# Kernel tuning notes

Hardware: AMD Instinct MI355X
Metric: run time of the kernel (lower is better)

The kernel has to match this reference:

```python
import jax, jax.numpy as jnp
import numpy as np

N = 250000          # number of points (also used as padded #unique voxels)
EPS = 1e-5          # BatchNorm1d eps
DIMS = [9, 64, 128, 256, 64]
PROJ = 16


def _bn(x, g, b):
    # torch BatchNorm1d in training mode: biased batch var
    m = jnp.mean(x, axis=0)
    v = jnp.var(x, axis=0)
    return (x - m) * jax.lax.rsqrt(v + EPS) * g + b


def setup_inputs() -> dict:
    key = jax.random.key(0)
    ks = list(jax.random.split(key, 24))
    inp = {
        "feats": jax.random.normal(ks[0], (N, DIMS[0]), jnp.float32),
        "coords": jax.random.randint(ks[1], (N, 3), 0, 48, jnp.int32),
    }
    k = 2
    # 4 BatchNorms over dims 9, 64, 128, 256
    for i, d in enumerate(DIMS[:4]):
        inp[f"bn{i}_g"] = jnp.ones((d,), jnp.float32)
        inp[f"bn{i}_b"] = jnp.zeros((d,), jnp.float32)
    # 4 Linear layers 9->64->128->256->64, stored as [in, out]
    for i in range(4):
        fin, fout = DIMS[i], DIMS[i + 1]
        inp[f"w{i+1}"] = jax.random.normal(ks[k], (fin, fout), jnp.float32) * (1.0 / np.sqrt(fin)); k += 1
        inp[f"b{i+1}"] = jnp.zeros((fout,), jnp.float32)
    # feature projection 64 -> 16 (kaiming-ish init, bias 0.01)
    inp["wp"] = jax.random.normal(ks[k], (DIMS[4], PROJ), jnp.float32) * np.sqrt(2.0 / PROJ); k += 1
    inp["bp"] = jnp.full((PROJ,), 0.01, jnp.float32)
    return inp


def reference(feats, coords, bn0_g, bn0_b, bn1_g, bn1_b, bn2_g, bn2_b, bn3_g, bn3_b,
              w1, b1, w2, b2, w3, b3, w4, b4, wp, bp):
    # unique voxel coords (sorted rows, like torch.unique dim=0); padded to N for jit
    unq, inv, cnt = jnp.unique(coords, axis=0, return_inverse=True, return_counts=True,
                               size=N, fill_value=-1)
    inv = inv.reshape(-1)

    # point MLP: BN -> Lin -> BN -> ReLU -> Lin -> BN -> ReLU -> Lin -> BN -> ReLU -> Lin
    x = _bn(feats, bn0_g, bn0_b)
    x = jax.nn.relu(_bn(x @ w1 + b1, bn1_g, bn1_b))
    x = jax.nn.relu(_bn(x @ w2 + b2, bn2_g, bn2_b))
    x = jax.nn.relu(_bn(x @ w3 + b3, bn3_g, bn3_b))
    x = x @ w4 + b4                                   # [N, 64]

    # scatter_max pooling per voxel; empty (padding) segments zeroed
    pooled = jax.ops.segment_max(x, inv, num_segments=N)
    pooled = jnp.where((cnt > 0)[:, None], pooled, 0.0)

    # feature projection + ReLU
    pooled = jax.nn.relu(pooled @ wp + bp)            # [N, 16] (rows >= #unique are padding)
    return pooled, unq.astype(jnp.int32)
```

## Files before the change

### kernel.cpp

```cpp
#include <hip/hip_runtime.h>
#include <hip/hip_bf16.h>

#define EPSBN 1e-5f
#define NKEYS 110592
#define SLICES 64
#define VPW 8

typedef __attribute__((ext_vector_type(8))) short bf16x8;
typedef __attribute__((ext_vector_type(4))) float f32x4;

__device__ __forceinline__ float bf2f(ushort u){ return __uint_as_float(((unsigned)u)<<16); }
__device__ __forceinline__ ushort f2bf(float f){
  unsigned u = __float_as_uint(f);
  unsigned r = u + 0x7fffu + ((u>>16)&1u);
  return (ushort)(r>>16);
}

template<int KP>
__device__ __forceinline__ int swz(int row, int kbyte){
  constexpr int MASK = (KP >= 64) ? 7 : 3;
  return row*(KP*2) + (kbyte ^ ((row & MASK) << 4));
}

__device__ __forceinline__ int tri(int k, int l){
  if (k > l){ int t=k; k=l; l=t; }
  return k*9 - (k*(k-1))/2 + (l-k);
}

__global__ __launch_bounds__(256) void k_zero(uint4* __restrict__ p, size_t n16){
  size_t i = (size_t)blockIdx.x*256 + threadIdx.x;
  size_t stride = (size_t)gridDim.x*256;
  uint4 z = make_uint4(0,0,0,0);
  for (; i < n16; i += stride) p[i] = z;
}

__global__ __launch_bounds__(256) void k_wprep(const float* __restrict__ w,
    ushort* __restrict__ wf, int K, int M){
  int CT = M >> 4;
  int KS = (K + 31) >> 5;
  int total = KS*CT*512;
  for (int idx = blockIdx.x*256 + threadIdx.x; idx < total; idx += gridDim.x*256){
    int e = idx & 7, l = (idx>>3) & 63, c = idx >> 9;
    int ct = c % CT, ks = c / CT;
    int g = l >> 4, j = l & 15;
    int k = ks*32 + g*8 + e, col = ct*16 + j;
    wf[idx] = (k < K) ? f2bf(w[(size_t)k*M + col]) : (ushort)0;
  }
}

__global__ __launch_bounds__(256) void k_keys(const int* __restrict__ coords,
    unsigned* __restrict__ cnt, int n){
  int i = blockIdx.x*256 + threadIdx.x;
  if (i >= n) return;
  int x = coords[3*i+0], y = coords[3*i+1], z = coords[3*i+2];
  atomicAdd(&cnt[(unsigned)((x*48 + y)*48 + z)], 1u);
}

__global__ __launch_bounds__(256) void k_scan1(const unsigned* __restrict__ cnt,
    unsigned* __restrict__ rloc, unsigned* __restrict__ ploc, unsigned* __restrict__ bsum){
  __shared__ unsigned tf[256], tc[256];
  int t = threadIdx.x;
  int base = blockIdx.x*1024 + t*4;
  uint4 cv = *(const uint4*)&cnt[base];
  unsigned f0 = cv.x?1u:0u, f1 = cv.y?1u:0u, f2 = cv.z?1u:0u, f3 = cv.w?1u:0u;
  unsigned sf = f0+f1+f2+f3;
  unsigned sc = cv.x+cv.y+cv.z+cv.w;
  tf[t] = sf; tc[t] = sc;
  __syncthreads();
  for (int off=1; off<256; off<<=1){
    unsigned af = (t>=off) ? tf[t-off] : 0u;
    unsigned ac = (t>=off) ? tc[t-off] : 0u;
    __syncthreads();
    tf[t] += af; tc[t] += ac;
    __syncthreads();
  }
  unsigned rf = tf[t] - sf, rc = tc[t] - sc;
  rloc[base+0] = rf; rf += f0;    ploc[base+0] = rc; rc += cv.x;
  rloc[base+1] = rf; rf += f1;    ploc[base+1] = rc; rc += cv.y;
  rloc[base+2] = rf; rf += f2;    ploc[base+2] = rc; rc += cv.z;
  rloc[base+3] = rf;              ploc[base+3] = rc;
  if (t == 255){ bsum[2*blockIdx.x] = tf[255]; bsum[2*blockIdx.x+1] = tc[255]; }
}

__global__ __launch_bounds__(128) void k_scan2(const unsigned* __restrict__ bsum,
    unsigned* __restrict__ boff){
  __shared__ unsigned tf[128], tc[128];
  int t = threadIdx.x;
  unsigned vf = (t < 108) ? bsum[2*t] : 0u;
  unsigned vc = (t < 108) ? bsum[2*t+1] : 0u;
  tf[t] = vf; tc[t] = vc;
  __syncthreads();
  for (int off=1; off<128; off<<=1){
    unsigned af = (t>=off) ? tf[t-off] : 0u;
    unsigned ac = (t>=off) ? tc[t-off] : 0u;
    __syncthreads();
    tf[t] += af; tc[t] += ac;
    __syncthreads();
  }
  boff[2*t] = tf[t] - vf;
  boff[2*t+1] = tc[t] - vc;
}

__global__ __launch_bounds__(256) void k_unq(const unsigned* __restrict__ cnt,
    const unsigned* __restrict__ rloc, const unsigned* __restrict__ ploc,
    const unsigned* __restrict__ boff, float* __restrict__ unq,
    unsigned* __restrict__ vst, unsigned* __restrict__ vct){
  int k = blockIdx.x*256 + threadIdx.x;
  if (k >= NKEYS) return;
  unsigned c = cnt[k];
  if (c == 0) return;
  unsigned r  = rloc[k] + boff[2*(k>>10)];
  unsigned st = ploc[k] + boff[2*(k>>10)+1];
  float z = (float)(k % 48);
  float y = (float)((k/48) % 48);
  float x = (float)(k / 2304);
  unq[3*(size_t)r+0] = x; unq[3*(size_t)r+1] = y; unq[3*(size_t)r+2] = z;
  vst[r] = st; vct[r] = c;
}

__global__ __launch_bounds__(256) void k_csr(const int* __restrict__ coords,
    const unsigned* __restrict__ ploc, const unsigned* __restrict__ boff,
    unsigned* __restrict__ cursor, unsigned* __restrict__ csr, int n){
  int i = blockIdx.x*256 + threadIdx.x;
  if (i >= n) return;
  int x = coords[3*i+0], y = coords[3*i+1], z = coords[3*i+2];
  unsigned k = (unsigned)((x*48 + y)*48 + z);
  unsigned slot = atomicAdd(&cursor[k], 1u);
  unsigned st = ploc[k] + boff[2*(k>>10)+1];
  csr[st + slot] = i;
}

__global__ __launch_bounds__(256) void k_stats0x(const float* __restrict__ X,
    float* __restrict__ slices, int n){
  float s[9], q[45];
  #pragma unroll
  for (int k=0;k<9;k++) s[k]=0.f;
  #pragma unroll
  for (int i=0;i<45;i++) q[i]=0.f;
  int stride = gridDim.x*256;
  for (int i = blockIdx.x*256 + threadIdx.x; i < n; i += stride){
    float v[9];
    #pragma unroll
    for (int k=0;k<9;k++) v[k] = X[(size_t)i*9+k];
    int qi=0;
    #pragma unroll
    for (int k=0;k<9;k++){
      s[k] += v[k];
      #pragma unroll
      for (int l=k;l<9;l++) q[qi++] += v[k]*v[l];
    }
  }
  #pragma unroll
  for (int off=32; off>0; off>>=1){
    #pragma unroll
    for (int k=0;k<9;k++)  s[k] += __shfl_down(s[k], off, 64);
    #pragma unroll
    for (int i=0;i<45;i++) q[i] += __shfl_down(q[i], off, 64);
  }
  if ((threadIdx.x & 63) == 0){
    float* sl = slices + (size_t)(blockIdx.x & (SLICES-1))*54;
    #pragma unroll
    for (int k=0;k<9;k++)  atomicAdd(&sl[k],   s[k]);
    #pragma unroll
    for (int i=0;i<45;i++) atomicAdd(&sl[9+i], q[i]);
  }
}

__global__ __launch_bounds__(256) void k_fin01(const float* __restrict__ slices, float invN,
    const float* __restrict__ g0, const float* __restrict__ b0,
    const float* __restrict__ g1, const float* __restrict__ b1,
    const float* __restrict__ w1, float* __restrict__ ac0, float* __restrict__ ac1){
  __shared__ float pa[4][64];
  __shared__ float red[54];
  __shared__ float ms[9], a0s[9], c0s[9];
  int t = threadIdx.x;
  {
    int col = t & 63, ch = t >> 6;
    float a = 0.f;
    if (col < 54){
      #pragma unroll 4
      for (int sl = ch*16; sl < ch*16 + 16; sl++) a += slices[(size_t)sl*54 + col];
    }
    pa[ch][col] = a;
  }
  __syncthreads();
  if (t < 54) red[t] = pa[0][t] + pa[1][t] + pa[2][t] + pa[3][t];
  __syncthreads();
  if (t < 9){
    float m = red[t]*invN;
    float var = red[9 + tri(t,t)]*invN - m*m;
    float a0 = g0[t]*rsqrtf(var + EPSBN);
    float c0 = b0[t] - m*a0;
    ms[t] = m; a0s[t] = a0; c0s[t] = c0;
    ac0[t] = a0; ac0[9+t] = c0;
  }
  __syncthreads();
  if (t < 64){
    float wj[9];
    #pragma unroll
    for (int k=0;k<9;k++) wj[k] = w1[(size_t)k*64 + t];
    float mean = 0.f;
    #pragma unroll
    for (int k=0;k<9;k++) mean += (ms[k]*a0s[k] + c0s[k])*wj[k];
    float e2 = 0.f;
    #pragma unroll
    for (int k=0;k<9;k++)
      #pragma unroll
      for (int l=0;l<9;l++){
        float U = a0s[k]*a0s[l]*(red[9 + tri(k,l)]*invN)
                + a0s[k]*c0s[l]*ms[k] + a0s[l]*c0s[k]*ms[l] + c0s[k]*c0s[l];
        e2 += wj[k]*wj[l]*U;
      }
    float var = e2 - mean*mean;
    float a = g1[t]*rsqrtf(var + EPSBN);
    ac1[t] = a;
    ac1[64+t] = b1[t] - mean*a;
  }
}

__global__ __launch_bounds__(256) void k_fin(const float* __restrict__ slices, int M, float invN,
    const float* __restrict__ g, const float* __restrict__ b, float* __restrict__ ac){
  __shared__ float ps[4][64], pss[4][64];
  int t = threadIdx.x;
  int col = t & 63, ch = t >> 6;
  int j = blockIdx.x*64 + col;
  float s = 0.f, ss = 0.f;
  #pragma unroll 4
  for (int sl = ch*16; sl < ch*16 + 16; sl++){
    s  += slices[(size_t)sl*2*M + j];
    ss += slices[(size_t)sl*2*M + M + j];
  }
  ps[ch][col] = s; pss[ch][col] = ss;
  __syncthreads();
  if (t < 64){
    j = blockIdx.x*64 + t;
    float S  = ps[0][t]+ps[1][t]+ps[2][t]+ps[3][t];
    float SS = pss[0][t]+pss[1][t]+pss[2][t]+pss[3][t];
    float mean = S*invN;
    float var = SS*invN - mean*mean;
    float a = g[j]*rsqrtf(var + EPSBN);
    ac[j] = a;
    ac[M+j] = b[j] - mean*a;
  }
}

__global__ __launch_bounds__(256,2) void k_chain12(
    const float* __restrict__ feats, const float* __restrict__ ac0,
    const ushort* __restrict__ w1f, const float* __restrict__ ac1,
    const ushort* __restrict__ w2f, const unsigned* __restrict__ csr,
    ushort* __restrict__ t2, float* __restrict__ slices, int n){
  __shared__ __align__(16) char smem[12288];
  __shared__ unsigned rid_s[64];
  char* X0 = smem;
  char* T1 = smem + 4096;
  int t = threadIdx.x;
  int lane = t & 63, w = t >> 6;
  int lrow = lane & 15, lgrp = lane >> 4;
  int rowbase = blockIdx.x * 64;

  bf16x8 b1 = *(const bf16x8*)(w1f + (size_t)(w*64 + lane)*8);
  if (t < 64){
    int gr = rowbase + t;
    rid_s[t] = (gr < n) ? csr[gr] : 0u;
  }
  __syncthreads();
  for (int e = t; e < 2048; e += 256){
    int row = e >> 5, k = e & 31;
    int gr = rowbase + row;
    float v = (k < 9 && gr < n) ? fmaf(feats[(size_t)rid_s[row]*9 + k], ac0[k], ac0[9+k]) : 0.f;
    *(ushort*)(X0 + swz<32>(row, k*2)) = f2bf(v);
  }
  __syncthreads();

  f32x4 acc0[4] = {};
  #pragma unroll
  for (int rb = 0; rb < 4; rb++){
    bf16x8 a = *(const bf16x8*)(X0 + swz<32>(rb*16 + lrow, lgrp*16));
    acc0[rb] = __builtin_amdgcn_mfma_f32_16x16x32_bf16(a, b1, acc0[rb], 0,0,0);
  }
  {
    int j = w*16 + lrow;
    float a1 = ac1[j], c1 = ac1[64+j];
    #pragma unroll
    for (int rb=0;rb<4;rb++)
      #pragma unroll
      for (int r=0;r<4;r++){
        int row = rb*16 + 4*lgrp + r;
        float v = fmaxf(fmaf(acc0[rb][r], a1, c1), 0.f);
        if (rowbase + row >= n) v = 0.f;
        *(ushort*)(T1 + swz<64>(row, j*2)) = f2bf(v);
      }
  }
  __syncthreads();

  f32x4 acc1[4][2] = {};
  #pragma unroll
  for (int ks=0; ks<2; ks++){
    bf16x8 bb[2];
    #pragma unroll
    for (int f=0;f<2;f++)
      bb[f] = *(const bf16x8*)(w2f + (size_t)((ks*8 + 2*w + f)*64 + lane)*8);
    #pragma unroll
    for (int rb=0;rb<4;rb++){
      bf16x8 a = *(const bf16x8*)(T1 + swz<64>(rb*16 + lrow, ks*64 + lgrp*16));
      #pragma unroll
      for (int f=0;f<2;f++)
        acc1[rb][f] = __builtin_amdgcn_mfma_f32_16x16x32_bf16(a, bb[f], acc1[rb][f], 0,0,0);
    }
  }

  float s[2]={0.f,0.f}, ss[2]={0.f,0.f};
  #pragma unroll
  for (int rb=0;rb<4;rb++)
    #pragma unroll
    for (int f=0;f<2;f++)
      #pragma unroll
      for (int r=0;r<4;r++){
        int gr = rowbase + rb*16 + 4*lgrp + r;
        if (gr < n){
          ushort h = f2bf(acc1[rb][f][r]);
          t2[(size_t)gr*128 + w*32 + 16*f + lrow] = h;
          float fr = bf2f(h);
          s[f] += fr; ss[f] += fr*fr;
        }
      }
  __syncthreads();
  float* ssum = (float*)smem;
  ssum[t] = 0.f;
  __syncthreads();
  #pragma unroll
  for (int f=0;f<2;f++){
    int j = w*32 + 16*f + lrow;
    atomicAdd(&ssum[j], s[f]); atomicAdd(&ssum[128+j], ss[f]);
  }
  __syncthreads();
  float* gsl = slices + (size_t)(blockIdx.x & (SLICES-1))*256;
  atomicAdd(&gsl[t], ssum[t]);
}

__device__ __forceinline__ void stage_T2(char* T2, const ushort* __restrict__ t2,
    const float* __restrict__ ac2, int rowbase, int t, int n){
  for (int e = t; e < 1024; e += 256){
    int row = e >> 4, k8 = (e & 15) << 3;
    int gr = rowbase + row;
    bf16x8 v = {};
    if (gr < n) v = *(const bf16x8*)(t2 + (size_t)gr*128 + k8);
    float4 A0 = *(const float4*)(ac2 + k8),       A1 = *(const float4*)(ac2 + k8 + 4);
    float4 C0 = *(const float4*)(ac2 + 128 + k8), C1 = *(const float4*)(ac2 + 128 + k8 + 4);
    float Av[8] = {A0.x,A0.y,A0.z,A0.w,A1.x,A1.y,A1.z,A1.w};
    float Cv[8] = {C0.x,C0.y,C0.z,C0.w,C1.x,C1.y,C1.z,C1.w};
    bf16x8 o;
    #pragma unroll
    for (int i=0;i<8;i++){
      float f = (gr < n) ? fmaxf(fmaf(bf2f((ushort)v[i]), Av[i], Cv[i]), 0.f) : 0.f;
      o[i] = f2bf(f);
    }
    *(bf16x8*)(T2 + swz<128>(row, k8*2)) = o;
  }
}

__global__ __launch_bounds__(256,2) void k_stage3(
    const ushort* __restrict__ t2, const float* __restrict__ ac2,
    const ushort* __restrict__ w3f, float* __restrict__ slices, int n){
  __shared__ __align__(16) char smem[16384];
  char* T2 = smem;
  int t = threadIdx.x;
  int lane = t & 63, w = t >> 6;
  int lrow = lane & 15, lgrp = lane >> 4;
  int rowbase = blockIdx.x * 64;
  stage_T2(T2, t2, ac2, rowbase, t, n);
  __syncthreads();

  f32x4 acc2[4][4] = {};
  #pragma unroll
  for (int ks=0; ks<4; ks++){
    bf16x8 bb[4];
    #pragma unroll
    for (int f=0;f<4;f++)
      bb[f] = *(const bf16x8*)(w3f + (size_t)((ks*16 + 4*w + f)*64 + lane)*8);
    #pragma unroll
    for (int rb=0;rb<4;rb++){
      bf16x8 a = *(const bf16x8*)(T2 + swz<128>(rb*16 + lrow, ks*64 + lgrp*16));
      #pragma unroll
      for (int f=0;f<4;f++)
        acc2[rb][f] = __builtin_amdgcn_mfma_f32_16x16x32_bf16(a, bb[f], acc2[rb][f], 0,0,0);
    }
  }
  __syncthreads();
  float* ssum = (float*)smem;
  for (int e=t; e<512; e+=256) ssum[e] = 0.f;
  __syncthreads();
  #pragma unroll
  for (int f=0;f<4;f++){
    float s=0.f, ss=0.f;
    #pragma unroll
    for (int rb=0;rb<4;rb++)
      #pragma unroll
      for (int r=0;r<4;r++){ float v=acc2[rb][f][r]; s+=v; ss+=v*v; }
    int j = 64*w + 16*f + lrow;
    atomicAdd(&ssum[j], s); atomicAdd(&ssum[256+j], ss);
  }
  __syncthreads();
  float* gsl = slices + (size_t)(blockIdx.x & (SLICES-1))*512;
  for (int e=t; e<512; e+=256) atomicAdd(&gsl[e], ssum[e]);
}

__global__ __launch_bounds__(256,2) void k_stage34(
    const ushort* __restrict__ t2, const float* __restrict__ ac2,
    const ushort* __restrict__ w3f, const float* __restrict__ ac3,
    const ushort* __restrict__ w4f, const float* __restrict__ b4,
    ushort* __restrict__ y4, int n){
  __shared__ __align__(16) char smem[32768];
  char* T2 = smem + 16384;
  char* X3 = smem;
  int t = threadIdx.x;
  int lane = t & 63, w = t >> 6;
  int lrow = lane & 15, lgrp = lane >> 4;
  int rowbase = blockIdx.x * 64;
  stage_T2(T2, t2, ac2, rowbase, t, n);
  __syncthreads();

  f32x4 acc2[4][4] = {};
  #pragma unroll
  for (int ks=0; ks<4; ks++){
    bf16x8 bb[4];
    #pragma unroll
    for (int f=0;f<4;f++)
      bb[f] = *(const bf16x8*)(w3f + (size_t)((ks*16 + 4*w + f)*64 + lane)*8);
    #pragma unroll
    for (int rb=0;rb<4;rb++){
      bf16x8 a = *(const bf16x8*)(T2 + swz<128>(rb*16 + lrow, ks*64 + lgrp*16));
      #pragma unroll
      for (int f=0;f<4;f++)
        acc2[rb][f] = __builtin_amdgcn_mfma_f32_16x16x32_bf16(a, bb[f], acc2[rb][f], 0,0,0);
    }
  }
  __syncthreads();

  #pragma unroll
  for (int f=0;f<4;f++){
    int j = 64*w + 16*f + lrow;
    float a3 = ac3[j], c3 = ac3[256+j];
    #pragma unroll
    for (int rb=0;rb<4;rb++)
      #pragma unroll
      for (int r=0;r<4;r++){
        int row = rb*16 + 4*lgrp + r;
        float v = fmaxf(fmaf(acc2[rb][f][r], a3, c3), 0.f);
        if (rowbase + row >= n) v = 0.f;
        *(ushort*)(X3 + swz<256>(row, j*2)) = f2bf(v);
      }
  }
  __syncthreads();

  f32x4 acc3[4] = {};
  #pragma unroll
  for (int ks=0; ks<8; ks++){
    bf16x8 b = *(const bf16x8*)(w4f + (size_t)((ks*4 + w)*64 + lane)*8);
    #pragma unroll
    for (int rb=0;rb<4;rb++){
      bf16x8 a = *(const bf16x8*)(X3 + swz<256>(rb*16 + lrow, ks*64 + lgrp*16));
      acc3[rb] = __builtin_amdgcn_mfma_f32_16x16x32_bf16(a, b, acc3[rb], 0,0,0);
    }
  }
  {
    int j = w*16 + lrow;
    float bias4 = b4[j];
    #pragma unroll
    for (int rb=0;rb<4;rb++)
      #pragma unroll
      for (int r=0;r<4;r++){
        int gr = rowbase + 16*rb + 4*lgrp + r;
        if (gr < n) y4[(size_t)gr*64 + j] = f2bf(acc3[rb][r] + bias4);
      }
  }
}

template<int DEPTH>
__global__ __launch_bounds__(256,2) void k_chain(
    const float* __restrict__ feats, const float* __restrict__ ac0,
    const ushort* __restrict__ w1f, const float* __restrict__ ac1,
    const ushort* __restrict__ w2f, const float* __restrict__ ac2,
    const ushort* __restrict__ w3f, const float* __restrict__ ac3,
    const ushort* __restrict__ w4f, const float* __restrict__ b4,
    const unsigned* __restrict__ csr, ushort* __restrict__ y4,
    float* __restrict__ slices, int n){
  constexpr int SMEM = (DEPTH==2) ? 12288 : (DEPTH==3) ? 28672 : 32768;
  __shared__ __align__(16) char smem[SMEM];
  __shared__ unsigned rid_s[64];
  char* X0 = smem;
  int t = threadIdx.x;
  int lane = t & 63, w = t >> 6;
  int lrow = lane & 15, lgrp = lane >> 4;
  int rowbase = blockIdx.x * 64;
  bf16x8 b1 = *(const bf16x8*)(w1f + (size_t)(w*64 + lane)*8);
  if constexpr (DEPTH == 4){
    if (t < 64){
      int gr = rowbase + t;
      rid_s[t] = (gr < n) ? csr[gr] : 0u;
    }
    __syncthreads();
  }
  for (int e = t; e < 2048; e += 256){
    int row = e >> 5, k = e & 31;
    int gr = rowbase + row;
    size_t rid = (DEPTH == 4) ? (size_t)rid_s[row] : (size_t)gr;
    float v = (k < 9 && gr < n) ? fmaf(feats[rid*9 + k], ac0[k], ac0[9+k]) : 0.f;
    *(ushort*)(X0 + swz<32>(row, k*2)) = f2bf(v);
  }
  __syncthreads();
  f32x4 acc0[4] = {};
  #pragma unroll
  for (int rb = 0; rb < 4; rb++){
    bf16x8 a = *(const bf16x8*)(X0 + swz<32>(rb*16 + lrow, lgrp*16));
    acc0[rb] = __builtin_amdgcn_mfma_f32_16x16x32_bf16(a, b1, acc0[rb], 0,0,0);
  }
  char* T1 = smem + 4096;
  {
    int j = w*16 + lrow;
    float a1 = ac1[j], c1 = ac1[64+j];
    #pragma unroll
    for (int rb=0;rb<4;rb++)
      #pragma unroll
      for (int r=0;r<4;r++){
        int row = rb*16 + 4*lgrp + r;
        float v = fmaxf(fmaf(acc0[rb][r], a1, c1), 0.f);
        if (rowbase + row >= n) v = 0.f;
        *(ushort*)(T1 + swz<64>(row, j*2)) = f2bf(v);
      }
  }
  __syncthreads();
  f32x4 acc1[4][2] = {};
  #pragma unroll
  for (int ks=0; ks<2; ks++){
    bf16x8 bb[2];
    #pragma unroll
    for (int f=0;f<2;f++)
      bb[f] = *(const bf16x8*)(w2f + (size_t)((ks*8 + 2*w + f)*64 + lane)*8);
    #pragma unroll
    for (int rb=0;rb<4;rb++){
      bf16x8 a = *(const bf16x8*)(T1 + swz<64>(rb*16 + lrow, ks*64 + lgrp*16));
      #pragma unroll
      for (int f=0;f<2;f++)
        acc1[rb][f] = __builtin_amdgcn_mfma_f32_16x16x32_bf16(a, bb[f], acc1[rb][f], 0,0,0);
    }
  }
  if constexpr (DEPTH == 2){
    float s[2]={0.f,0.f}, ss[2]={0.f,0.f};
    #pragma unroll
    for (int rb=0;rb<4;rb++)
      #pragma unroll
      for (int f=0;f<2;f++)
        #pragma unroll
        for (int r=0;r<4;r++){ float v=acc1[rb][f][r]; s[f]+=v; ss[f]+=v*v; }
    __syncthreads();
    float* ssum = (float*)smem;
    ssum[t] = 0.f;
    __syncthreads();
    #pragma unroll
    for (int f=0;f<2;f++){
      int j = w*32 + 16*f + lrow;
      atomicAdd(&ssum[j], s[f]); atomicAdd(&ssum[128+j], ss[f]);
    }
    __syncthreads();
    float* gsl = slices + (size_t)(blockIdx.x & (SLICES-1))*256;
    atomicAdd(&gsl[t], ssum[t]);
    return;
  }
  if constexpr (DEPTH >= 3){
  char* T2 = smem + 12288;
  #pragma unroll
  for (int f=0;f<2;f++){
    int j = w*32 + 16*f + lrow;
    float a2 = ac2[j], c2 = ac2[128+j];
    #pragma unroll
    for (int rb=0;rb<4;rb++)
      #pragma unroll
      for (int r=0;r<4;r++){
        int row = rb*16 + 4*lgrp + r;
        float v = fmaxf(fmaf(acc1[rb][f][r], a2, c2), 0.f);
        if (rowbase + row >= n) v = 0.f;
        *(ushort*)(T2 + swz<128>(row, j*2)) = f2bf(v);
      }
  }
  __syncthreads();
  if constexpr (DEPTH == 3){
    float s3[2][2], ss3[2][2];
    #pragma unroll
    for (int h=0; h<2; h++){
      f32x4 acc2[4][2] = {};
      #pragma unroll
      for (int ks=0; ks<4; ks++){
        bf16x8 bb[2];
        #pragma unroll
        for (int f=0;f<2;f++)
          bb[f] = *(const bf16x8*)(w3f + (size_t)((ks*16 + 4*w + 2*h + f)*64 + lane)*8);
        #pragma unroll
        for (int rb=0;rb<4;rb++){
          bf16x8 a = *(const bf16x8*)(T2 + swz<128>(rb*16 + lrow, ks*64 + lgrp*16));
          #pragma unroll
          for (int f=0;f<2;f++)
            acc2[rb][f] = __builtin_amdgcn_mfma_f32_16x16x32_bf16(a, bb[f], acc2[rb][f], 0,0,0);
        }
      }
      #pragma unroll
      for (int f=0;f<2;f++){
        float s=0.f, ss=0.f;
        #pragma unroll
        for (int rb=0;rb<4;rb++)
          #pragma unroll
          for (int r=0;r<4;r++){ float v=acc2[rb][f][r]; s+=v; ss+=v*v; }
        s3[h][f]=s; ss3[h][f]=ss;
      }
    }
    __syncthreads();
    float* ssum = (float*)smem;
    for (int e=t; e<512; e+=256) ssum[e] = 0.f;
    __syncthreads();
    #pragma unroll
    for (int h=0;h<2;h++)
      #pragma unroll
      for (int f=0;f<2;f++){
        int j = 64*w + 32*h + 16*f + lrow;
        atomicAdd(&ssum[j], s3[h][f]); atomicAdd(&ssum[256+j], ss3[h][f]);
      }
    __syncthreads();
    float* gsl = slices + (size_t)(blockIdx.x & (SLICES-1))*512;
    for (int e=t; e<512; e+=256) atomicAdd(&gsl[e], ssum[e]);
    return;
  }
  if constexpr (DEPTH == 4){
  f32x4 acc2[4][4] = {};
  #pragma unroll
  for (int ks=0; ks<4; ks++){
    bf16x8 bb[4];
    #pragma unroll
    for (int f=0;f<4;f++)
      bb[f] = *(const bf16x8*)(w3f + (size_t)((ks*16 + 4*w + f)*64 + lane)*8);
    #pragma unroll
    for (int rb=0;rb<4;rb++){
      bf16x8 a = *(const bf16x8*)(T2 + swz<128>(rb*16 + lrow, ks*64 + lgrp*16));
      #pragma unroll
      for (int f=0;f<4;f++)
        acc2[rb][f] = __builtin_amdgcn_mfma_f32_16x16x32_bf16(a, bb[f], acc2[rb][f], 0,0,0);
    }
  }
  __syncthreads();
  char* X3 = smem;
  #pragma unroll
  for (int f=0;f<4;f++){
    int j = 64*w + 16*f + lrow;
    float a3 = ac3[j], c3 = ac3[256+j];
    #pragma unroll
    for (int rb=0;rb<4;rb++)
      #pragma unroll
      for (int r=0;r<4;r++){
        int row = rb*16 + 4*lgrp + r;
        float v = fmaxf(fmaf(acc2[rb][f][r], a3, c3), 0.f);
        if (rowbase + row >= n) v = 0.f;
        *(ushort*)(X3 + swz<256>(row, j*2)) = f2bf(v);
      }
  }
  __syncthreads();
  f32x4 acc3[4] = {};
  #pragma unroll
  for (int ks=0; ks<8; ks++){
    bf16x8 b = *(const bf16x8*)(w4f + (size_t)((ks*4 + w)*64 + lane)*8);
    #pragma unroll
    for (int rb=0;rb<4;rb++){
      bf16x8 a = *(const bf16x8*)(X3 + swz<256>(rb*16 + lrow, ks*64 + lgrp*16));
      acc3[rb] = __builtin_amdgcn_mfma_f32_16x16x32_bf16(a, b, acc3[rb], 0,0,0);
    }
  }
  {
    int j = w*16 + lrow;
    float bias4 = b4[j];
    #pragma unroll
    for (int rb=0;rb<4;rb++)
      #pragma unroll
      for (int r=0;r<4;r++){
        int gr = rowbase + 16*rb + 4*lgrp + r;
        if (gr < n){
          y4[(size_t)gr*64 + j] = f2bf(acc3[rb][r] + bias4);
        }
      }
  }
  }
  }
}

__global__ __launch_bounds__(256) void k_pool(const ushort* __restrict__ y4,
    const unsigned* __restrict__ vst, const unsigned* __restrict__ vct,
    const unsigned* __restrict__ boff, const float* __restrict__ wp,
    const float* __restrict__ bp, float* __restrict__ out, int n){
  __shared__ float wpsT[1024];
  __shared__ float sm[4][64];
  int t = threadIdx.x, w = t >> 6, lane = t & 63;
  for (int e=t; e<1024; e+=256){
    int j = e >> 6, ch = e & 63;
    wpsT[e] = wp[ch*16 + j];
  }
  __syncthreads();
  unsigned M = boff[216];
  int base = blockIdx.x*(4*VPW) + w*VPW;
  if (base >= (int)M) return;
  float bpv = (lane < 16) ? bp[lane] : 0.f;
  int q = lane >> 4, j = lane & 15;
  int vend = (int)M - base; if (vend > VPW) vend = VPW;
  for (int v = 0; v < vend; v++){
    int r = base + v;
    unsigned st = vst[r], c = vct[r];
    const ushort* row = y4 + (size_t)st*64 + lane;
    float m = bf2f(row[0]);
    #pragma unroll 4
    for (unsigned pp = 1; pp < c; pp++)
      m = fmaxf(m, bf2f(row[(size_t)pp*64]));
    sm[w][lane] = m;
    float acc = 0.f;
    #pragma unroll
    for (int i=0;i<16;i++) acc = fmaf(sm[w][q*16+i], wpsT[j*64 + q*16+i], acc);
    acc += __shfl_xor(acc, 16, 64);
    acc += __shfl_xor(acc, 32, 64);
    if (lane < 16) out[(size_t)r*16 + lane] = fmaxf(acc + bpv, 0.f);
  }
}

__global__ __launch_bounds__(256) void k_fill(const unsigned* __restrict__ boff,
    const float* __restrict__ bp, float* __restrict__ out,
    float* __restrict__ unq, int n){
  int r = blockIdx.x*256 + threadIdx.x;
  if (r >= n) return;
  unsigned M = boff[216];
  if ((unsigned)r < M) return;
  #pragma unroll
  for (int j=0;j<16;j++) out[(size_t)r*16 + j] = fmaxf(bp[j], 0.f);
  unq[3*(size_t)r+0] = -1.f; unq[3*(size_t)r+1] = -1.f; unq[3*(size_t)r+2] = -1.f;
}

extern "C" void kernel_launch(void* const* d_in, const int* in_sizes, int n_in,
                              void* d_out, int out_size, void* d_ws, size_t ws_size,
                              hipStream_t stream){
  (void)n_in; (void)out_size;
  const float* feats  = (const float*)d_in[0];
  const int*   coords = (const int*)d_in[1];
  const float* g0=(const float*)d_in[2];  const float* bb0=(const float*)d_in[3];
  const float* g1=(const float*)d_in[4];  const float* bb1=(const float*)d_in[5];
  const float* g2=(const float*)d_in[6];  const float* bb2=(const float*)d_in[7];
  const float* g3=(const float*)d_in[8];  const float* bb3=(const float*)d_in[9];
  const float* w1=(const float*)d_in[10];
  const float* w2=(const float*)d_in[12];
  const float* w3=(const float*)d_in[14];
  const float* w4=(const float*)d_in[16]; const float* b4=(const float*)d_in[17];
  const float* wp=(const float*)d_in[18]; const float* bp=(const float*)d_in[19];
  int n = in_sizes[0]/9;

  char* ws = (char*)d_ws;
  size_t off = 0;
  auto alloc = [&](size_t bytes){ size_t o = off; off = (off + bytes + 255) & ~(size_t)255; return o; };
  size_t o_cnt  = alloc((size_t)NKEYS*4);
  size_t o_cur  = alloc((size_t)NKEYS*4);
  size_t o_sl0  = alloc((size_t)SLICES*54*4);
  size_t o_sl2  = alloc((size_t)SLICES*256*4);
  size_t o_sl3  = alloc((size_t)SLICES*512*4);
  size_t zero_end = off;
  size_t o_rloc = alloc((size_t)NKEYS*4);
  size_t o_ploc = alloc((size_t)NKEYS*4);
  size_t o_bsum = alloc(256*4);
  size_t o_boff = alloc(256*4);
  size_t o_ac0  = alloc(18*4);
  size_t o_ac1  = alloc(128*4);
  size_t o_ac2  = alloc(256*4);
  size_t o_ac3  = alloc(512*4);
  size_t o_w1f  = alloc(2048*2);
  size_t o_w2f  = alloc(8192*2);
  size_t o_w3f  = alloc(32768*2);
  size_t o_w4f  = alloc(16384*2);
  size_t o_csr  = alloc((size_t)n*4);
  size_t o_vst  = alloc((size_t)n*4);
  size_t o_vct  = alloc((size_t)n*4);
  size_t o_y4   = alloc((size_t)n*64*2);
  size_t off_base = off;
  size_t o_t2   = alloc((size_t)n*128*2);
  size_t off_full = off;
  if (ws_size < off_base) return;
  bool bigws = (ws_size >= off_full);

  unsigned* cnt  = (unsigned*)(ws + o_cnt);
  unsigned* cursor = (unsigned*)(ws + o_cur);
  unsigned* rloc = (unsigned*)(ws + o_rloc);
  unsigned* ploc = (unsigned*)(ws + o_ploc);
  unsigned* bsum = (unsigned*)(ws + o_bsum);
  unsigned* boff = (unsigned*)(ws + o_boff);
  float* sl0 = (float*)(ws + o_sl0);
  float* sl2 = (float*)(ws + o_sl2);
  float* sl3 = (float*)(ws + o_sl3);
  float* ac0 = (float*)(ws + o_ac0);
  float* ac1 = (float*)(ws + o_ac1);
  float* ac2 = (float*)(ws + o_ac2);
  float* ac3 = (float*)(ws + o_ac3);
  ushort* w1f = (ushort*)(ws + o_w1f);
  ushort* w2f = (ushort*)(ws + o_w2f);
  ushort* w3f = (ushort*)(ws + o_w3f);
  ushort* w4f = (ushort*)(ws + o_w4f);
  unsigned* csr = (unsigned*)(ws + o_csr);
  unsigned* vst = (unsigned*)(ws + o_vst);
  unsigned* vct = (unsigned*)(ws + o_vct);
  ushort* y4 = (ushort*)(ws + o_y4);
  ushort* t2 = (ushort*)(ws + o_t2);

  float* out_pool = (float*)d_out;
  float* out_unq  = out_pool + (size_t)n*16;

  {
    size_t n16 = zero_end/16;
    int zb = (int)((n16 + 255)/256); if (zb > 2048) zb = 2048;
    k_zero<<<zb,256,0,stream>>>((uint4*)ws, n16);
  }

  k_wprep<<<8,256,0,stream>>>(w1, w1f, 9, 64);
  k_wprep<<<32,256,0,stream>>>(w2, w2f, 64, 128);
  k_wprep<<<128,256,0,stream>>>(w3, w3f, 128, 256);
  k_wprep<<<64,256,0,stream>>>(w4, w4f, 256, 64);

  int nb = (n + 255)/256;
  k_keys<<<nb,256,0,stream>>>(coords, cnt, n);
  k_scan1<<<NKEYS/1024,256,0,stream>>>(cnt, rloc, ploc, bsum);
  k_scan2<<<1,128,0,stream>>>(bsum, boff);
  k_unq<<<(NKEYS+255)/256,256,0,stream>>>(cnt, rloc, ploc, boff, out_unq, vst, vct);
  k_csr<<<nb,256,0,stream>>>(coords, ploc, boff, cursor, csr, n);

  k_stats0x<<<512,256,0,stream>>>(feats, sl0, n);
  k_fin01<<<1,256,0,stream>>>(sl0, 1.f/(float)n, g0, bb0, g1, bb1, w1, ac0, ac1);

  int gb = (n+63)/64;
  if (bigws){
    k_chain12<<<gb,256,0,stream>>>(feats, ac0, w1f, ac1, w2f, csr, t2, sl2, n);
    k_fin<<<2,256,0,stream>>>(sl2, 128, 1.f/(float)n, g2, bb2, ac2);
    k_stage3<<<gb,256,0,stream>>>(t2, ac2, w3f, sl3, n);
    k_fin<<<4,256,0,stream>>>(sl3, 256, 1.f/(float)n, g3, bb3, ac3);
    k_stage34<<<gb,256,0,stream>>>(t2, ac2, w3f, ac3, w4f, b4, y4, n);
  } else {
    k_chain<2><<<gb,256,0,stream>>>(feats, ac0, w1f, ac1, w2f, ac2, w3f, ac3, w4f, b4, nullptr, nullptr, sl2, n);
    k_fin<<<2,256,0,stream>>>(sl2, 128, 1.f/(float)n, g2, bb2, ac2);
    k_chain<3><<<gb,256,0,stream>>>(feats, ac0, w1f, ac1, w2f, ac2, w3f, ac3, w4f, b4, nullptr, nullptr, sl3, n);
    k_fin<<<4,256,0,stream>>>(sl3, 256, 1.f/(float)n, g3, bb3, ac3);
    k_chain<4><<<gb,256,0,stream>>>(feats, ac0, w1f, ac1, w2f, ac2, w3f, ac3, w4f, b4, csr, y4, nullptr, n);
  }

  int maxv = (n < NKEYS) ? n : NKEYS;
  k_pool<<<(maxv + 4*VPW - 1)/(4*VPW),256,0,stream>>>(y4, vst, vct, boff, wp, bp, out_pool, n);
  k_fill<<<nb,256,0,stream>>>(boff, bp, out_pool, out_unq, n);
}
```

Before: 289.3 us.

## Materialize layer-3 activations to avoid recomputing the 128x256 GEMM

Stage 3 now writes its bf16 pre-BN outputs to a new workspace buffer t3 and takes its BN statistics from the rounded values. A new k_stage4 kernel reads t3, applies BN3+ReLU, and runs only the 256->64 GEMM, so the 128->256 GEMM is no longer computed twice. In exchange it writes and re-reads 128 MB of bf16 data (N x 256 x 2 bytes each way), and its scattered 2-byte stores from the MFMA accumulator layout may coalesce poorly. It is only used when the workspace is large enough.

```diff
diff --git a/kernel.cpp b/kernel.cpp
--- a/kernel.cpp
+++ b/kernel.cpp
@@ -359,9 +359,11 @@
   }
 }
 
+template<int STORET3>
 __global__ __launch_bounds__(256,2) void k_stage3(
     const ushort* __restrict__ t2, const float* __restrict__ ac2,
-    const ushort* __restrict__ w3f, float* __restrict__ slices, int n){
+    const ushort* __restrict__ w3f, ushort* __restrict__ t3,
+    float* __restrict__ slices, int n){
   __shared__ __align__(16) char smem[16384];
   char* T2 = smem;
   int t = threadIdx.x;
@@ -392,17 +394,82 @@
   __syncthreads();
   #pragma unroll
   for (int f=0;f<4;f++){
+    int j = 64*w + 16*f + lrow;
     float s=0.f, ss=0.f;
     #pragma unroll
     for (int rb=0;rb<4;rb++)
       #pragma unroll
-      for (int r=0;r<4;r++){ float v=acc2[rb][f][r]; s+=v; ss+=v*v; }
-    int j = 64*w + 16*f + lrow;
+      for (int r=0;r<4;r++){
+        if constexpr (STORET3){
+          int gr = rowbase + rb*16 + 4*lgrp + r;
+          if (gr < n){
+            ushort h = f2bf(acc2[rb][f][r]);
+            t3[(size_t)gr*256 + j] = h;
+            float v = bf2f(h);
+            s += v; ss += v*v;
+          }
+        } else {
+          float v = acc2[rb][f][r]; s += v; ss += v*v;
+        }
+      }
     atomicAdd(&ssum[j], s); atomicAdd(&ssum[256+j], ss);
   }
   __syncthreads();
   float* gsl = slices + (size_t)(blockIdx.x & (SLICES-1))*512;
   for (int e=t; e<512; e+=256) atomicAdd(&gsl[e], ssum[e]);
+}
+
+__global__ __launch_bounds__(256,2) void k_stage4(
+    const ushort* __restrict__ t3, const float* __restrict__ ac3,
+    const ushort* __restrict__ w4f, const float* __restrict__ b4,
+    ushort* __restrict__ y4, int n){
+  __shared__ __align__(16) char smem[32768];
+  char* X3 = smem;
+  int t = threadIdx.x;
+  int lane = t & 63, w = t >> 6;
+  int lrow = lane & 15, lgrp = lane >> 4;
+  int rowbase = blockIdx.x * 64;
+
+  for (int e = t; e < 2048; e += 256){
+    int row = e >> 5, k8 = (e & 31) << 3;
+    int gr = rowbase + row;
+    bf16x8 v = {};
+    if (gr < n) v = *(const bf16x8*)(t3 + (size_t)gr*256 + k8);
+    float4 A0 = *(const float4*)(ac3 + k8),       A1 = *(const float4*)(ac3 + k8 + 4);
+    float4 C0 = *(const float4*)(ac3 + 256 + k8), C1 = *(const float4*)(ac3 + 256 + k8 + 4);
+    float Av[8] = {A0.x,A0.y,A0.z,A0.w,A1.x,A1.y,A1.z,A1.w};
+    float Cv[8] = {C0.x,C0.y,C0.z,C0.w,C1.x,C1.y,C1.z,C1.w};
+    bf16x8 o;
+    #pragma unroll
+    for (int i=0;i<8;i++){
+      float f = (gr < n) ? fmaxf(fmaf(bf2f((ushort)v[i]), Av[i], Cv[i]), 0.f) : 0.f;
+      o[i] = f2bf(f);
+    }
+    *(bf16x8*)(X3 + swz<256>(row, k8*2)) = o;
+  }
+  __syncthreads();
+
+  f32x4 acc3[4] = {};
+  #pragma unroll
+  for (int ks=0; ks<8; ks++){
+    bf16x8 b = *(const bf16x8*)(w4f + (size_t)((ks*4 + w)*64 + lane)*8);
+    #pragma unroll
+    for (int rb=0;rb<4;rb++){
+      bf16x8 a = *(const bf16x8*)(X3 + swz<256>(rb*16 + lrow, ks*64 + lgrp*16));
+      acc3[rb] = __builtin_amdgcn_mfma_f32_16x16x32_bf16(a, b, acc3[rb], 0,0,0);
+    }
+  }
+  {
+    int j = w*16 + lrow;
+    float bias4 = b4[j];
+    #pragma unroll
+    for (int rb=0;rb<4;rb++)
+      #pragma unroll
+      for (int r=0;r<4;r++){
+        int gr = rowbase + 16*rb + 4*lgrp + r;
+        if (gr < n) y4[(size_t)gr*64 + j] = f2bf(acc3[rb][r] + bias4);
+      }
+  }
 }
 
 __global__ __launch_bounds__(256,2) void k_stage34(
@@ -782,8 +849,11 @@
   size_t off_base = off;
   size_t o_t2   = alloc((size_t)n*128*2);
   size_t off_full = off;
+  size_t o_t3   = alloc((size_t)n*256*2);
+  size_t off_full2 = off;
   if (ws_size < off_base) return;
-  bool bigws = (ws_size >= off_full);
+  bool bigws  = (ws_size >= off_full);
+  bool bigws2 = (ws_size >= off_full2);
 
   unsigned* cnt  = (unsigned*)(ws + o_cnt);
   unsigned* cursor = (unsigned*)(ws + o_cur);
@@ -807,6 +877,7 @@
   unsigned* vct = (unsigned*)(ws + o_vct);
   ushort* y4 = (ushort*)(ws + o_y4);
   ushort* t2 = (ushort*)(ws + o_t2);
+  ushort* t3 = (ushort*)(ws + o_t3);
 
   float* out_pool = (float*)d_out;
   float* out_unq  = out_pool + (size_t)n*16;
@@ -836,9 +907,15 @@
   if (bigws){
     k_chain12<<<gb,256,0,stream>>>(feats, ac0, w1f, ac1, w2f, csr, t2, sl2, n);
     k_fin<<<2,256,0,stream>>>(sl2, 128, 1.f/(float)n, g2, bb2, ac2);
-    k_stage3<<<gb,256,0,stream>>>(t2, ac2, w3f, sl3, n);
-    k_fin<<<4,256,0,stream>>>(sl3, 256, 1.f/(float)n, g3, bb3, ac3);
-    k_stage34<<<gb,256,0,stream>>>(t2, ac2, w3f, ac3, w4f, b4, y4, n);
+    if (bigws2){
+      k_stage3<1><<<gb,256,0,stream>>>(t2, ac2, w3f, t3, sl3, n);
+      k_fin<<<4,256,0,stream>>>(sl3, 256, 1.f/(float)n, g3, bb3, ac3);
+      k_stage4<<<gb,256,0,stream>>>(t3, ac3, w4f, b4, y4, n);
+    } else {
+      k_stage3<0><<<gb,256,0,stream>>>(t2, ac2, w3f, nullptr, sl3, n);
+      k_fin<<<4,256,0,stream>>>(sl3, 256, 1.f/(float)n, g3, bb3, ac3);
+      k_stage34<<<gb,256,0,stream>>>(t2, ac2, w3f, ac3, w4f, b4, y4, n);
+    }
   } else {
     k_chain<2><<<gb,256,0,stream>>>(feats, ac0, w1f, ac1, w2f, ac2, w3f, ac3, w4f, b4, nullptr, nullptr, sl2, n);
     k_fin<<<2,256,0,stream>>>(sl2, 128, 1.f/(float)n, g2, bb2, ac2);
```

Result: slower. 300.2 us (+3.8%).
